# Kernel optimization log

Hardware: AMD Instinct MI355X
Metric: run time of the kernel (lower is better)

The kernel has to match this reference:

```python
import jax, jax.numpy as jnp
import numpy as np

N_STATE = 2048
N_HEAD = 16
HEAD_DIM = N_STATE // N_HEAD  # 128
ROPE_THETA = 10000.0


def setup_inputs() -> dict:
    key = jax.random.key(0)
    ks = jax.random.split(key, 8)
    B, S, D = 2, 2048, N_STATE
    scale = 1.0 / np.sqrt(D)
    x = jax.random.normal(ks[0], (B, S, D), dtype=jnp.float32)
    Wq = jax.random.normal(ks[1], (D, D), dtype=jnp.float32) * scale
    bq = jnp.zeros((D,), dtype=jnp.float32)
    Wk = jax.random.normal(ks[2], (D, D), dtype=jnp.float32) * scale  # key has no bias
    Wv = jax.random.normal(ks[3], (D, D), dtype=jnp.float32) * scale
    bv = jnp.zeros((D,), dtype=jnp.float32)
    Wo = jax.random.normal(ks[4], (D, D), dtype=jnp.float32) * scale
    bo = jnp.zeros((D,), dtype=jnp.float32)
    return {"x": x, "Wq": Wq, "bq": bq, "Wk": Wk, "Wv": Wv, "bv": bv, "Wo": Wo, "bo": bo}


def _rope(t, pos):
    # t: [B, S, H, hd]; torchtune-style interleaved rotary (pairs of adjacent dims)
    hd = t.shape[-1]
    inv_freq = 1.0 / (ROPE_THETA ** (jnp.arange(0, hd, 2, dtype=jnp.float32) / hd))  # [hd/2]
    ang = pos[:, None] * inv_freq[None, :]                    # [S, hd/2]
    cos = jnp.cos(ang)[None, :, None, :].astype(t.dtype)       # [1,S,1,hd/2]
    sin = jnp.sin(ang)[None, :, None, :].astype(t.dtype)
    t1 = t[..., 0::2]
    t2 = t[..., 1::2]
    rot = jnp.stack([t1 * cos - t2 * sin, t2 * cos + t1 * sin], axis=-1)
    return rot.reshape(t.shape)


def reference(x, Wq, bq, Wk, Wv, bv, Wo, bo):
    B, S, D = x.shape
    H, hd = N_HEAD, D // N_HEAD
    q = (x @ Wq.T + bq).reshape(B, S, H, hd)
    k = (x @ Wk.T).reshape(B, S, H, hd)
    v = (x @ Wv.T + bv).reshape(B, S, H, hd)
    pos = jnp.arange(S, dtype=jnp.float32)
    q = _rope(q, pos)
    k = _rope(k, pos)
    # [B,H,S,hd]
    q = q.transpose(0, 2, 1, 3)
    k = k.transpose(0, 2, 1, 3)
    v = v.transpose(0, 2, 1, 3)
    scale = 1.0 / jnp.sqrt(jnp.asarray(hd, dtype=x.dtype))
    scores = jnp.einsum('bhqd,bhkd->bhqk', q, k) * scale       # [B,H,S,S]
    causal = jnp.tril(jnp.ones((S, S), dtype=bool))
    scores = jnp.where(causal[None, None], scores, jnp.finfo(scores.dtype).min)
    probs = jax.nn.softmax(scores, axis=-1)
    a = jnp.einsum('bhqk,bhkd->bhqd', probs, v)                # [B,H,S,hd]
    a = a.transpose(0, 2, 1, 3).reshape(B, S, D)
    return a @ Wo.T + bo
```

## Files before the change

kernel.cpp:

```cpp
#include <hip/hip_runtime.h>
#include <stdint.h>

typedef float f32x4 __attribute__((ext_vector_type(4)));
typedef __bf16 bf16x8 __attribute__((ext_vector_type(8)));
typedef unsigned short us8 __attribute__((ext_vector_type(8)));
typedef unsigned short us4 __attribute__((ext_vector_type(4)));
typedef unsigned int u32;

#define MFMA16(A, B, C) __builtin_amdgcn_mfma_f32_16x16x32_bf16( \
    __builtin_bit_cast(bf16x8, (A)), __builtin_bit_cast(bf16x8, (B)), (C), 0, 0, 0)

__device__ __forceinline__ unsigned short f2bf(float f) {
  u32 u = __builtin_bit_cast(u32, f);
  u = u + 0x7fffu + ((u >> 16) & 1u);
  return (unsigned short)(u >> 16);
}
__device__ __forceinline__ float bf2f(unsigned short b) {
  u32 u = ((u32)b) << 16;
  return __builtin_bit_cast(float, u);
}
__device__ __forceinline__ void gload16(const void* g, void* lds) {
  __builtin_amdgcn_global_load_lds((const __attribute__((address_space(1))) u32*)g,
                                   (__attribute__((address_space(3))) u32*)lds, 16, 0, 0);
}

__global__ __launch_bounds__(256) void convert_all(
    const float* __restrict__ x, const float* __restrict__ wq, const float* __restrict__ wk,
    const float* __restrict__ wv, const float* __restrict__ wo,
    unsigned short* __restrict__ xb, unsigned short* __restrict__ wcat,
    unsigned short* __restrict__ wob, float2* __restrict__ tab) {
  if (blockIdx.x >= 2048) {
    int t0 = ((int)blockIdx.x - 2048) * 2048 + (int)threadIdx.x * 8;
#pragma unroll
    for (int j = 0; j < 8; ++j) {
      int idx = t0 + j;
      int s = idx >> 6, i = idx & 63;
      float ang = (float)s * exp2f(-(float)i * 0.2076205059304703f);
      float sv, cv;
      sincosf(ang, &sv, &cv);
      tab[idx] = make_float2(cv, sv);
    }
    return;
  }
  int tid = blockIdx.x * 256 + threadIdx.x;
  int nth = 2048 * 256;
  const float* srcs[5] = {x, wq, wk, wv, wo};
  unsigned short* dsts[5] = {xb, wcat, wcat + 4194304, wcat + 8388608, wob};
  const int n4s[5] = {2097152, 1048576, 1048576, 1048576, 1048576};
#pragma unroll
  for (int sg = 0; sg < 5; ++sg) {
    const float4* s = (const float4*)srcs[sg];
    us4* d = (us4*)dsts[sg];
    int n4 = n4s[sg];
    for (int i = tid; i < n4; i += nth) {
      float4 v = s[i];
      us4 o;
      o[0] = f2bf(v.x); o[1] = f2bf(v.y); o[2] = f2bf(v.z); o[3] = f2bf(v.w);
      d[i] = o;
    }
  }
}

template <int EPI>
__global__ __launch_bounds__(512, 2) void gemmsw(
    const unsigned short* __restrict__ A, const unsigned short* __restrict__ B,
    int nTN, int N,
    float* __restrict__ outF, const float* __restrict__ bias,
    unsigned short* __restrict__ qb, unsigned short* __restrict__ kb,
    unsigned short* __restrict__ vtb, const float* __restrict__ bq,
    const float* __restrict__ bv, const float2* __restrict__ tab) {
  constexpr int KT = 32;
  __shared__ alignas(16) char L[114688];
  char* Lp = L;
  int bid = (int)blockIdx.x, nwg = (int)gridDim.x;
  {
    int qq = nwg >> 3;
    int xcd = bid & 7, idx = bid >> 3;
    bid = xcd * qq + idx;
  }
  int tm = bid / nTN, tn = bid % nTN;
  int t = (int)threadIdx.x, l = t & 63, w = t >> 6;
  int g = l >> 4, ln = l & 15;
  int wr = w >> 2, wc = w & 3;
  int lr = l >> 3, lc = l & 7;
  int scol = lc ^ lr;
  const unsigned short* pAs = A + (size_t)(tm * 256 + w * 8 + lr) * 2048 + scol * 8;
  const unsigned short* pBs = B + (size_t)(tn * 192 + w * 8 + lr) * 2048 + scol * 8;

  f32x4 acc[2][3][4] = {};
  us8 af[2][4][2], bf[2];

#define FENCE asm volatile("" ::: "memory")
#define BAR do { FENCE; __builtin_amdgcn_s_barrier(); FENCE; } while (0)
#define VMW_(n) asm volatile("s_waitcnt vmcnt(" #n ")" ::: "memory")
#define VMW(n) VMW_(n)
#define STA(i, kt, bufsel) do { if ((kt) < KT)                                \
    gload16(pAs + (size_t)(i) * 131072 + (size_t)(kt) * 64,                   \
            Lp + (bufsel) * 57344 + (i) * 8192 + w * 1024); } while (0)
#define STB(i, kt, bufsel) do { if ((kt) < KT)                                \
    gload16(pBs + (size_t)(i) * 131072 + (size_t)(kt) * 64,                   \
            Lp + (bufsel) * 57344 + 32768 + (i) * 8192 + w * 1024); } while (0)
#define RD_AALL(bufsel) do {                                                  \
    _Pragma("unroll") for (int mh = 0; mh < 2; ++mh)                          \
    _Pragma("unroll") for (int mf = 0; mf < 4; ++mf)                          \
    _Pragma("unroll") for (int kc = 0; kc < 2; ++kc)                          \
      af[mh][mf][kc] = *(const us8*)(Lp + (bufsel) * 57344 +                  \
          (wr * 128 + mh * 64 + mf * 16 + ln) * 128 +                         \
          ((kc * 64 + g * 16) ^ ((ln & 7) << 4)));                            \
  } while (0)
#define RD_B(nh_, bufsel) do {                                                \
    _Pragma("unroll") for (int kc = 0; kc < 2; ++kc)                          \
      bf[kc] = *(const us8*)(Lp + (bufsel) * 57344 + 32768 +                  \
          ((nh_) * 64 + wc * 16 + ln) * 128 +                                 \
          ((kc * 64 + g * 16) ^ ((ln & 7) << 4)));                            \
  } while (0)
#define MMF(nh_) do {                                                         \
    __builtin_amdgcn_s_setprio(1);                                            \
    _Pragma("unroll") for (int kc = 0; kc < 2; ++kc)                          \
    _Pragma("unroll") for (int mh = 0; mh < 2; ++mh)                          \
    _Pragma("unroll") for (int mf = 0; mf < 4; ++mf)                          \
      acc[mh][nh_][mf] = MFMA16(af[mh][mf][kc], bf[kc], acc[mh][nh_][mf]);    \
    __builtin_amdgcn_s_setprio(0);                                            \
  } while (0)
#define TILE(kt, b, VM0, VM1, VMB) do {                                       \
   RD_AALL(b); RD_B(0, b);                                             \
          STA(0, (kt) + 1, (b) ^ 1); STA(1, (kt) + 1, (b) ^ 1);               \
          STA(2, (kt) + 1, (b) ^ 1); STA(3, (kt) + 1, (b) ^ 1);               \
          STB(0, (kt) + 1, (b) ^ 1);                                          \
          BAR; MMF(0); VMW(VM0); BAR;                                         \
   RD_B(1, b);                                                         \
          STB(1, (kt) + 1, (b) ^ 1);                                          \
          BAR; MMF(1); VMW(VM1); BAR;                                         \
   RD_B(2, b);                                                         \
          STB(2, (kt) + 1, (b) ^ 1);                                          \
          MMF(2); VMW(VMB); BAR;                                              \
} while (0)

  STA(0, 0, 0); STA(1, 0, 0); STA(2, 0, 0); STA(3, 0, 0); STB(0, 0, 0);
  STB(1, 0, 0); STB(2, 0, 0);
  VMW(2); BAR;

#pragma unroll 1
  for (int kt = 0; kt < 30; kt += 2) {
    TILE(kt, 0, 6, 6, 2);
    TILE(kt + 1, 1, 6, 6, 2);
  }
  TILE(30, 0, 6, 6, 2);
  TILE(31, 1, 1, 0, 0);

#undef TILE
#undef MMF
#undef RD_B
#undef RD_AALL
#undef STB
#undef STA
#undef VMW
#undef VMW_
#undef BAR
#undef FENCE

  if (EPI == 1) {
#pragma unroll
    for (int mh = 0; mh < 2; ++mh)
#pragma unroll
    for (int nh = 0; nh < 3; ++nh)
#pragma unroll
    for (int mf = 0; mf < 4; ++mf) {
      int n = tn * 192 + nh * 64 + wc * 16 + ln;
      float bz = bias[n];
      int m0 = tm * 256 + wr * 128 + mh * 64 + mf * 16 + g * 4;
#pragma unroll
      for (int r = 0; r < 4; ++r)
        outF[(size_t)(m0 + r) * N + n] = acc[mh][nh][mf][r] + bz;
    }
  } else {
#pragma unroll
    for (int mh = 0; mh < 2; ++mh)
#pragma unroll
    for (int nh = 0; nh < 3; ++nh)
#pragma unroll
    for (int mf = 0; mf < 4; ++mf) {
      int n6 = tn * 192 + nh * 64 + wc * 16 + ln;
      int sel = n6 >> 11, d = n6 & 2047, h = d >> 7, hd = d & 127;
      int m0 = tm * 256 + wr * 128 + mh * 64 + mf * 16 + g * 4;
      int b = m0 >> 11, s0 = m0 & 2047;
      if (sel == 2) {
        float badd = bv[d];
        us4 pk;
#pragma unroll
        for (int r = 0; r < 4; ++r) pk[r] = f2bf(acc[mh][nh][mf][r] + badd);
        *(us4*)&vtb[((size_t)(b * 16 + h) * 128 + hd) * 2048 + s0] = pk;
      } else {
        unsigned short* dst = sel ? kb : qb;
        float badd = sel ? 0.f : bq[d];
        int odd = hd & 1;
#pragma unroll
        for (int r = 0; r < 4; ++r) {
          float val = acc[mh][nh][mf][r] + badd;
          float pv = __shfl_xor(val, 1);
          float2 cs = tab[((s0 + r) << 6) | (hd >> 1)];
          float rot = odd ? (val * cs.x + pv * cs.y) : (val * cs.x - pv * cs.y);
          dst[((size_t)(b * 16 + h) * 2048 + (s0 + r)) * 128 + hd] = f2bf(rot);
        }
      }
    }
  }
}

__global__ __launch_bounds__(512, 2) void gemmo(
    const unsigned short* __restrict__ A, const unsigned short* __restrict__ B,
    int nTN, int N,
    float* __restrict__ outF, const float* __restrict__ bias) {
  constexpr int KT = 32;
  __shared__ alignas(16) char L[147456];
  char* Lp = L;
  int bid = (int)blockIdx.x, nwg = (int)gridDim.x;
  {
    int qq = nwg >> 3;
    int xcd = bid & 7, idx = bid >> 3;
    bid = xcd * qq + idx;
  }
  int tm = bid / nTN, tn = bid % nTN;
  int t = (int)threadIdx.x, l = t & 63, w = t >> 6;
  int g = l >> 4, ln = l & 15;
  int wr = w >> 2, wc = w & 3;
  int lr = l >> 3, lc = l & 7;
  int scol = lc ^ lr;
  const unsigned short* pAs = A + (size_t)(tm * 128 + w * 8 + lr) * 2048 + scol * 8;
  const unsigned short* pBs = B + (size_t)(tn * 256 + w * 8 + lr) * 2048 + scol * 8;

  f32x4 acc[4][4] = {};
  us8 af[4][2], bfp[2][2];

#define FENCE asm volatile("" ::: "memory")
#define BAR do { FENCE; __builtin_amdgcn_s_barrier(); FENCE; } while (0)
#define VMW_(n) asm volatile("s_waitcnt vmcnt(" #n ")" ::: "memory")
#define VMW(n) VMW_(n)
#define OSTA(i, kt, bufsel) do { if ((kt) < KT)                               \
    gload16(pAs + (size_t)(i) * 131072 + (size_t)(kt) * 64,                   \
            Lp + (bufsel) * 49152 + (i) * 8192 + w * 1024); } while (0)
#define OSTB(i, kt, bufsel) do { if ((kt) < KT)                               \
    gload16(pBs + (size_t)(i) * 131072 + (size_t)(kt) * 64,                   \
            Lp + (bufsel) * 49152 + 16384 + (i) * 8192 + w * 1024); } while (0)
#define ORD_A(bufsel) do {                                                    \
    _Pragma("unroll") for (int mf = 0; mf < 4; ++mf)                          \
    _Pragma("unroll") for (int kc = 0; kc < 2; ++kc)                          \
      af[mf][kc] = *(const us8*)(Lp + (bufsel) * 49152 +                      \
          (wr * 64 + mf * 16 + ln) * 128 +                                    \
          ((kc * 64 + g * 16) ^ ((ln & 7) << 4)));                            \
  } while (0)
#define ORD_B2(ph, bufsel) do {                                               \
    _Pragma("unroll") for (int np = 0; np < 2; ++np)                          \
    _Pragma("unroll") for (int kc = 0; kc < 2; ++kc)                          \
      bfp[np][kc] = *(const us8*)(Lp + (bufsel) * 49152 + 16384 +             \
          (((ph) * 2 + np) * 64 + wc * 16 + ln) * 128 +                       \
          ((kc * 64 + g * 16) ^ ((ln & 7) << 4)));                            \
  } while (0)
#define OMM(ph) do {                                                          \
    __builtin_amdgcn_s_setprio(1);                                            \
    _Pragma("unroll") for (int np = 0; np < 2; ++np)                          \
    _Pragma("unroll") for (int kc = 0; kc < 2; ++kc)                          \
    _Pragma("unroll") for (int mf = 0; mf < 4; ++mf)                          \
      acc[(ph) * 2 + np][mf] = MFMA16(af[mf][kc], bfp[np][kc],                \
                                      acc[(ph) * 2 + np][mf]);                \
    __builtin_amdgcn_s_setprio(0);                                            \
  } while (0)
#define OTILE(kt, bc, bs, VMB) do {                                           \
   ORD_A(bc); ORD_B2(0, bc);                                           \
          OSTA(0, (kt) + 2, bs); OSTA(1, (kt) + 2, bs);                       \
          OSTB(0, (kt) + 2, bs); OSTB(1, (kt) + 2, bs);                       \
          OSTB(2, (kt) + 2, bs); OSTB(3, (kt) + 2, bs);                       \
          BAR; OMM(0); BAR;                                                   \
   ORD_B2(1, bc); OMM(1); VMW(VMB); BAR;                               \
} while (0)

  OSTA(0, 0, 0); OSTA(1, 0, 0); OSTB(0, 0, 0); OSTB(1, 0, 0);
  OSTB(2, 0, 0); OSTB(3, 0, 0);
  OSTA(0, 1, 1); OSTA(1, 1, 1); OSTB(0, 1, 1); OSTB(1, 1, 1);
  OSTB(2, 1, 1); OSTB(3, 1, 1);
  VMW(6); BAR;

#pragma unroll 1
  for (int j = 0; j < 10; ++j) {
    int k0 = j * 3;
    OTILE(k0 + 0, 0, 2, 6);
    OTILE(k0 + 1, 1, 0, 6);
    OTILE(k0 + 2, 2, 1, 6);
  }
  OTILE(30, 0, 2, 0);
  OTILE(31, 1, 0, 0);

#undef OTILE
#undef OMM
#undef ORD_B2
#undef ORD_A
#undef OSTB
#undef OSTA
#undef VMW
#undef VMW_
#undef BAR
#undef FENCE

#pragma unroll
  for (int nh = 0; nh < 4; ++nh)
#pragma unroll
  for (int mf = 0; mf < 4; ++mf) {
    int n = tn * 256 + nh * 64 + wc * 16 + ln;
    float bz = bias[n];
    int m0 = tm * 128 + wr * 64 + mf * 16 + g * 4;
#pragma unroll
    for (int r = 0; r < 4; ++r)
      outF[(size_t)(m0 + r) * N + n] = acc[nh][mf][r] + bz;
  }
}

__global__ __launch_bounds__(512) void attn_k(
    const unsigned short* __restrict__ qg, const unsigned short* __restrict__ kg,
    const unsigned short* __restrict__ vtg, unsigned short* __restrict__ ab) {
  __shared__ alignas(16) unsigned short Kl[2][64 * 128];
  __shared__ alignas(16) unsigned short Vl[2][128 * 64];
  __shared__ alignas(16) unsigned short Pl[8][16 * 72];
  int bh = (int)blockIdx.x & 31;
  int pr = (int)blockIdx.x >> 5;
  int t = (int)threadIdx.x, l = t & 63, w = t >> 6;
  int g = l >> 4, ln = l & 15;
  int b = bh >> 4, h = bh & 15;
  const size_t bq0 = (size_t)bh * 2048 * 128;

  const int qbA = pr * 128, qbB = (15 - pr) * 128;
  const int qrowA = qbA + w * 16 + ln, qrowB = qbB + w * 16 + ln;
  us8 qfA[4], qfB[4];
#pragma unroll
  for (int kf = 0; kf < 4; ++kf) {
    qfA[kf] = *(const us8*)&qg[bq0 + (size_t)qrowA * 128 + kf * 32 + g * 8];
    qfB[kf] = *(const us8*)&qg[bq0 + (size_t)qrowB * 128 + kf * 32 + g * 8];
  }
  f32x4 oA[8] = {}, oB[8] = {};
  float mA = -1e30f, lA = 0.f, mB = -1e30f, lB = 0.f;
  const int nktA = (qbA >> 6) + 2;
  const int nkt  = (qbB >> 6) + 2;

#define STAGEKV(kt1, bsel) do {                                               \
    _Pragma("unroll") for (int i = 0; i < 2; ++i) {                           \
      int fb = i * 8192 + w * 1024;                                           \
      int flat = fb + l * 16;                                                 \
      int row = flat >> 8, colb = flat & 255;                                 \
      int sc = colb ^ ((row & 7) << 4);                                       \
      gload16(kg + (bq0 + (size_t)((kt1) * 64 + row) * 128 + (sc >> 1)),      \
              (char*)Kl + (bsel) * 16384 + fb);                               \
      int rv = flat >> 7, cv2 = flat & 127;                                   \
      int scv = cv2 ^ ((rv & 7) << 4);                                        \
      gload16(vtg + (bq0 + (size_t)rv * 2048 + (kt1) * 64 + (scv >> 1)),      \
              (char*)Vl + (bsel) * 16384 + fb);                               \
    }                                                                         \
  } while (0)

#define COMPUTE(qf, o, mrow, lrow, qrow, kt, bo) do {                         \
    f32x4 st[4];                                                              \
    _Pragma("unroll") for (int kfr = 0; kfr < 4; ++kfr) {                     \
      f32x4 acc = {};                                                         \
      int row = kfr * 16 + ln;                                                \
      int swz = (row & 7) << 4;                                               \
      _Pragma("unroll") for (int kf = 0; kf < 4; ++kf) {                      \
        us8 kfrag = *(const us8*)((const char*)Kl + (bo) + row * 256 +        \
                                  ((kf * 64 + g * 16) ^ swz));                \
        acc = MFMA16(kfrag, qf[kf], acc);                                     \
      }                                                                       \
      st[kfr] = acc;                                                          \
    }                                                                         \
    float pmax = -1e30f;                                                      \
    _Pragma("unroll") for (int kfr = 0; kfr < 4; ++kfr)                       \
    _Pragma("unroll") for (int r = 0; r < 4; ++r) {                           \
      int key = (kt) * 64 + kfr * 16 + g * 4 + r;                             \
      float sv = key <= (qrow) ? st[kfr][r] * 0.08838834764831845f : -1e30f;  \
      st[kfr][r] = sv;                                                        \
      pmax = fmaxf(pmax, sv);                                                 \
    }                                                                         \
    pmax = fmaxf(pmax, __shfl_xor(pmax, 16));                                 \
    pmax = fmaxf(pmax, __shfl_xor(pmax, 32));                                 \
    if (__ballot(pmax > (mrow) + 8.f)) {                                      \
      float mnew = pmax > (mrow) + 8.f ? pmax : (mrow);                       \
      float corr = exp2f(((mrow) - mnew) * 1.44269504f);                      \
      (mrow) = mnew;                                                          \
      (lrow) *= corr;                                                         \
      _Pragma("unroll") for (int r = 0; r < 4; ++r) {                         \
        float cr = __shfl(corr, g * 4 + r);                                   \
        _Pragma("unroll") for (int nf = 0; nf < 8; ++nf) o[nf][r] *= cr;      \
      }                                                                       \
    }                                                                         \
    float lsum = 0.f;                                                         \
    _Pragma("unroll") for (int kfr = 0; kfr < 4; ++kfr) {                     \
      us4 pk;                                                                 \
      _Pragma("unroll") for (int r = 0; r < 4; ++r) {                         \
        float p = exp2f((st[kfr][r] - (mrow)) * 1.44269504f);                 \
        lsum += p;                                                            \
        pk[r] = f2bf(p);                                                      \
      }                                                                       \
      *(us4*)&Pl[w][ln * 72 + kfr * 16 + g * 4] = pk;                         \
    }                                                                         \
    lsum += __shfl_xor(lsum, 16);                                             \
    lsum += __shfl_xor(lsum, 32);                                             \
    (lrow) += lsum;                                                           \
    _Pragma("unroll") for (int kf2 = 0; kf2 < 2; ++kf2) {                     \
      us8 pa = *(const us8*)&Pl[w][ln * 72 + kf2 * 32 + g * 8];               \
      _Pragma("unroll") for (int nf = 0; nf < 8; ++nf) {                      \
        int row = nf * 16 + ln;                                               \
        us8 vb = *(const us8*)((const char*)Vl + (bo) + row * 128 +           \
                               ((kf2 * 64 + g * 16) ^ ((row & 7) << 4)));     \
        o[nf] = MFMA16(pa, vb, o[nf]);                                        \
      }                                                                       \
    }                                                                         \
  } while (0)

  STAGEKV(0, 0);
#pragma unroll 1
  for (int kt = 0; kt < nkt; ++kt) {
    __syncthreads();
    if (kt + 1 < nkt) STAGEKV(kt + 1, (kt + 1) & 1);
    int bo = (kt & 1) * 16384;
    COMPUTE(qfB, oB, mB, lB, qrowB, kt, bo);
    if (kt < nktA) COMPUTE(qfA, oA, mA, lA, qrowA, kt, bo);
  }
#undef COMPUTE
#undef STAGEKV

  {
    float invl = 1.f / lB;
#pragma unroll
    for (int r = 0; r < 4; ++r) {
      float ir = __shfl(invl, g * 4 + r);
      int srow = qbB + w * 16 + g * 4 + r;
      size_t base = ((size_t)b * 2048 + srow) * 2048 + h * 128 + ln;
#pragma unroll
      for (int nf = 0; nf < 8; ++nf) ab[base + (size_t)nf * 16] = f2bf(oB[nf][r] * ir);
    }
  }
  {
    float invl = 1.f / lA;
#pragma unroll
    for (int r = 0; r < 4; ++r) {
      float ir = __shfl(invl, g * 4 + r);
      int srow = qbA + w * 16 + g * 4 + r;
      size_t base = ((size_t)b * 2048 + srow) * 2048 + h * 128 + ln;
#pragma unroll
      for (int nf = 0; nf < 8; ++nf) ab[base + (size_t)nf * 16] = f2bf(oA[nf][r] * ir);
    }
  }
}

extern "C" void kernel_launch(void* const* d_in, const int* in_sizes, int n_in,
                              void* d_out, int out_size, void* d_ws, size_t ws_size,
                              hipStream_t stream) {
  const float* x  = (const float*)d_in[0];
  const float* Wq = (const float*)d_in[1];
  const float* bq = (const float*)d_in[2];
  const float* Wk = (const float*)d_in[3];
  const float* Wv = (const float*)d_in[4];
  const float* bv = (const float*)d_in[5];
  const float* Wo = (const float*)d_in[6];
  const float* bo = (const float*)d_in[7];
  float* out = (float*)d_out;

  unsigned short* ws = (unsigned short*)d_ws;
  unsigned short* xb   = ws;
  unsigned short* wcat = xb + 8388608;
  unsigned short* wob  = wcat + 12582912;
  unsigned short* qb   = wob + 4194304;
  unsigned short* kb   = qb + 8388608;
  unsigned short* vtb  = kb + 8388608;
  float2* tab = (float2*)(vtb + 8388608);

  convert_all<<<2112, 256, 0, stream>>>(x, Wq, Wk, Wv, Wo, xb, wcat, wob, tab);
  gemmsw<0><<<512, 512, 0, stream>>>(xb, wcat, 32, 6144,
                                     nullptr, nullptr, qb, kb, vtb, bq, bv, tab);
  attn_k<<<256, 512, 0, stream>>>(qb, kb, vtb, xb );
  gemmo<<<256, 512, 0, stream>>>(xb, wob, 8, 2048, out, bo);
}
```

Before: 249.0 us.

## Share K and V fragment loads between both query tiles in attention loop

Restructures the attention inner loop so that each K fragment read from shared memory feeds MFMAs for both query blocks A and B, and each V fragment likewise serves both PV products. The softmax step is split into its own macro that runs per block between the two matmul phases. This halves LDS reads for K/V and interleaves independent MFMA chains. In exchange it keeps more registers live (two score tiles, two P fragments) and adds per-MFMA branches on doA, which may raise register pressure and lower occupancy.

```diff
diff --git a/kernel.cpp b/kernel.cpp
--- a/kernel.cpp
+++ b/kernel.cpp
@@ -355,19 +355,7 @@
     }                                                                         \
   } while (0)
 
-#define COMPUTE(qf, o, mrow, lrow, qrow, kt, bo) do {                         \
-    f32x4 st[4];                                                              \
-    _Pragma("unroll") for (int kfr = 0; kfr < 4; ++kfr) {                     \
-      f32x4 acc = {};                                                         \
-      int row = kfr * 16 + ln;                                                \
-      int swz = (row & 7) << 4;                                               \
-      _Pragma("unroll") for (int kf = 0; kf < 4; ++kf) {                      \
-        us8 kfrag = *(const us8*)((const char*)Kl + (bo) + row * 256 +        \
-                                  ((kf * 64 + g * 16) ^ swz));                \
-        acc = MFMA16(kfrag, qf[kf], acc);                                     \
-      }                                                                       \
-      st[kfr] = acc;                                                          \
-    }                                                                         \
+#define SMAXH(st, o, mrow, lrow, qrow, kt, pa) do {                           \
     float pmax = -1e30f;                                                      \
     _Pragma("unroll") for (int kfr = 0; kfr < 4; ++kfr)                       \
     _Pragma("unroll") for (int r = 0; r < 4; ++r) {                           \
@@ -401,15 +389,8 @@
     lsum += __shfl_xor(lsum, 16);                                             \
     lsum += __shfl_xor(lsum, 32);                                             \
     (lrow) += lsum;                                                           \
-    _Pragma("unroll") for (int kf2 = 0; kf2 < 2; ++kf2) {                     \
-      us8 pa = *(const us8*)&Pl[w][ln * 72 + kf2 * 32 + g * 8];               \
-      _Pragma("unroll") for (int nf = 0; nf < 8; ++nf) {                      \
-        int row = nf * 16 + ln;                                               \
-        us8 vb = *(const us8*)((const char*)Vl + (bo) + row * 128 +           \
-                               ((kf2 * 64 + g * 16) ^ ((row & 7) << 4)));     \
-        o[nf] = MFMA16(pa, vb, o[nf]);                                        \
-      }                                                                       \
-    }                                                                         \
+    pa[0] = *(const us8*)&Pl[w][ln * 72 + g * 8];                             \
+    pa[1] = *(const us8*)&Pl[w][ln * 72 + 32 + g * 8];                        \
   } while (0)
 
   STAGEKV(0, 0);
@@ -417,11 +398,39 @@
   for (int kt = 0; kt < nkt; ++kt) {
     __syncthreads();
     if (kt + 1 < nkt) STAGEKV(kt + 1, (kt + 1) & 1);
-    int bo = (kt & 1) * 16384;
-    COMPUTE(qfB, oB, mB, lB, qrowB, kt, bo);
-    if (kt < nktA) COMPUTE(qfA, oA, mA, lA, qrowA, kt, bo);
-  }
-#undef COMPUTE
+    const char* Kb = (const char*)Kl + (kt & 1) * 16384;
+    const char* Vb = (const char*)Vl + (kt & 1) * 16384;
+    bool doA = kt < nktA;
+    f32x4 stB[4], stA[4];
+#pragma unroll
+    for (int kfr = 0; kfr < 4; ++kfr) {
+      f32x4 aB = {}, aA = {};
+      int row = kfr * 16 + ln;
+      int swz = (row & 7) << 4;
+#pragma unroll
+      for (int kf = 0; kf < 4; ++kf) {
+        us8 kfrag = *(const us8*)(Kb + row * 256 + ((kf * 64 + g * 16) ^ swz));
+        aB = MFMA16(kfrag, qfB[kf], aB);
+        if (doA) aA = MFMA16(kfrag, qfA[kf], aA);
+      }
+      stB[kfr] = aB;
+      stA[kfr] = aA;
+    }
+    us8 paB[2], paA[2] = {};
+    SMAXH(stB, oB, mB, lB, qrowB, kt, paB);
+    if (doA) SMAXH(stA, oA, mA, lA, qrowA, kt, paA);
+#pragma unroll
+    for (int kf2 = 0; kf2 < 2; ++kf2)
+#pragma unroll
+      for (int nf = 0; nf < 8; ++nf) {
+        int row = nf * 16 + ln;
+        us8 vb = *(const us8*)(Vb + row * 128 +
+                               ((kf2 * 64 + g * 16) ^ ((row & 7) << 4)));
+        oB[nf] = MFMA16(paB[kf2], vb, oB[nf]);
+        if (doA) oA[nf] = MFMA16(paA[kf2], vb, oA[nf]);
+      }
+  }
+#undef SMAXH
 #undef STAGEKV
 
   {
```

New measurement: 798.1 us. 221% more time.

## Simplify GEMM main loop to a single barrier per K-tile

Applied to the files above, without the earlier changes.

Replaces the three-phase interleaved GEMM K-loop with a simpler schedule. Each tile now issues all global-to-LDS loads for the next tile, reads every A and B fragment from LDS, runs all MFMAs, then waits on all outstanding loads and hits a single barrier. The goal is fewer barriers and waitcnt stalls per tile. In exchange it drops the finer overlap of LDS reads with MFMAs across the three N-slices, waits for all loads every tile, and holds more B-fragment registers.

```diff
diff --git a/kernel.cpp b/kernel.cpp
--- a/kernel.cpp
+++ b/kernel.cpp
@@ -88,7 +88,7 @@
   const unsigned short* pBs = B + (size_t)(tn * 192 + w * 8 + lr) * 2048 + scol * 8;
 
   f32x4 acc[2][3][4] = {};
-  us8 af[2][4][2], bf[2];
+  us8 af[2][4][2], bf3[3][2];
 
 #define FENCE asm volatile("" ::: "memory")
 #define BAR do { FENCE; __builtin_amdgcn_s_barrier(); FENCE; } while (0)
@@ -108,49 +108,45 @@
           (wr * 128 + mh * 64 + mf * 16 + ln) * 128 +                         \
           ((kc * 64 + g * 16) ^ ((ln & 7) << 4)));                            \
   } while (0)
-#define RD_B(nh_, bufsel) do {                                                \
-    _Pragma("unroll") for (int kc = 0; kc < 2; ++kc)                          \
-      bf[kc] = *(const us8*)(Lp + (bufsel) * 57344 + 32768 +                  \
-          ((nh_) * 64 + wc * 16 + ln) * 128 +                                 \
+#define RD_BALL(bufsel) do {                                                  \
+    _Pragma("unroll") for (int nh = 0; nh < 3; ++nh)                          \
+    _Pragma("unroll") for (int kc = 0; kc < 2; ++kc)                          \
+      bf3[nh][kc] = *(const us8*)(Lp + (bufsel) * 57344 + 32768 +             \
+          (nh * 64 + wc * 16 + ln) * 128 +                                    \
           ((kc * 64 + g * 16) ^ ((ln & 7) << 4)));                            \
   } while (0)
-#define MMF(nh_) do {                                                         \
+#define MMALL() do {                                                          \
     __builtin_amdgcn_s_setprio(1);                                            \
+    _Pragma("unroll") for (int nh = 0; nh < 3; ++nh)                          \
     _Pragma("unroll") for (int kc = 0; kc < 2; ++kc)                          \
     _Pragma("unroll") for (int mh = 0; mh < 2; ++mh)                          \
     _Pragma("unroll") for (int mf = 0; mf < 4; ++mf)                          \
-      acc[mh][nh_][mf] = MFMA16(af[mh][mf][kc], bf[kc], acc[mh][nh_][mf]);    \
+      acc[mh][nh][mf] = MFMA16(af[mh][mf][kc], bf3[nh][kc], acc[mh][nh][mf]); \
     __builtin_amdgcn_s_setprio(0);                                            \
   } while (0)
-#define TILE(kt, b, VM0, VM1, VMB) do {                                       \
-   RD_AALL(b); RD_B(0, b);                                             \
-          STA(0, (kt) + 1, (b) ^ 1); STA(1, (kt) + 1, (b) ^ 1);               \
-          STA(2, (kt) + 1, (b) ^ 1); STA(3, (kt) + 1, (b) ^ 1);               \
-          STB(0, (kt) + 1, (b) ^ 1);                                          \
-          BAR; MMF(0); VMW(VM0); BAR;                                         \
-   RD_B(1, b);                                                         \
-          STB(1, (kt) + 1, (b) ^ 1);                                          \
-          BAR; MMF(1); VMW(VM1); BAR;                                         \
-   RD_B(2, b);                                                         \
-          STB(2, (kt) + 1, (b) ^ 1);                                          \
-          MMF(2); VMW(VMB); BAR;                                              \
+#define TILE1(kt, b) do {                                                     \
+  STA(0, (kt) + 1, (b) ^ 1); STA(1, (kt) + 1, (b) ^ 1);                       \
+  STA(2, (kt) + 1, (b) ^ 1); STA(3, (kt) + 1, (b) ^ 1);                       \
+  STB(0, (kt) + 1, (b) ^ 1); STB(1, (kt) + 1, (b) ^ 1);                       \
+  STB(2, (kt) + 1, (b) ^ 1);                                                  \
+  RD_AALL(b); RD_BALL(b);                                                     \
+  MMALL();                                                                    \
+  VMW(0); BAR;                                                                \
 } while (0)
 
-  STA(0, 0, 0); STA(1, 0, 0); STA(2, 0, 0); STA(3, 0, 0); STB(0, 0, 0);
-  STB(1, 0, 0); STB(2, 0, 0);
-  VMW(2); BAR;
+  STA(0, 0, 0); STA(1, 0, 0); STA(2, 0, 0); STA(3, 0, 0);
+  STB(0, 0, 0); STB(1, 0, 0); STB(2, 0, 0);
+  VMW(0); BAR;
 
 #pragma unroll 1
-  for (int kt = 0; kt < 30; kt += 2) {
-    TILE(kt, 0, 6, 6, 2);
-    TILE(kt + 1, 1, 6, 6, 2);
-  }
-  TILE(30, 0, 6, 6, 2);
-  TILE(31, 1, 1, 0, 0);
-
-#undef TILE
-#undef MMF
-#undef RD_B
+  for (int kt = 0; kt < 32; kt += 2) {
+    TILE1(kt, 0);
+    TILE1(kt + 1, 1);
+  }
+
+#undef TILE1
+#undef MMALL
+#undef RD_BALL
 #undef RD_AALL
 #undef STB
 #undef STA
```

Result: no change. 253.1 us (+1.6%).
